# Optimization experiments

Measured on AMD Instinct MI355X. Metric: run time of the kernel, lower is better.

The kernel has to match this reference:

```python
import jax, jax.numpy as jnp
import numpy as np

B, C, H, W = 4, 64, 64, 64
C8 = C // 8


def cl_attention(x, gamma):
    # DANet CAM-style channel attention: [B,C,H,W] -> [B,C,H,W]
    b, c, h, w = x.shape
    xf = x.reshape(b, c, h * w)                       # b c n
    energy = jnp.einsum('bcn,bdn->bcd', xf, xf)       # b c c
    energy = jnp.max(energy, axis=-1, keepdims=True) - energy
    attn = jax.nn.softmax(energy, axis=-1)
    out = jnp.einsum('bcd,bdn->bcn', attn, xf).reshape(b, c, h, w)
    return gamma * out + x


def setup_inputs() -> dict:
    key = jax.random.key(0)
    ks = jax.random.split(key, 8)
    s = 0.02
    return {
        'cnn_feat': jax.random.normal(ks[0], (B, C, H, W), jnp.float32),
        'vit_feat': jax.random.normal(ks[1], (B, C, H, W), jnp.float32),
        'Wq': jax.random.normal(ks[2], (C8, C), jnp.float32) * s,   # 1x1 conv kernel
        'bq': jnp.zeros((C8,), jnp.float32),
        'Wk': jax.random.normal(ks[3], (C8, C), jnp.float32) * s,
        'bk': jnp.zeros((C8,), jnp.float32),
        'Wv': jax.random.normal(ks[4], (C, C), jnp.float32) * s,
        'bv': jnp.zeros((C,), jnp.float32),
        'gamma': jnp.zeros((1,), jnp.float32),
        'gamma_cla_cnn': jnp.zeros((1,), jnp.float32),
        'gamma_cla_vit': jnp.zeros((1,), jnp.float32),
    }


def reference(cnn_feat, vit_feat, Wq, bq, Wk, bk, Wv, bv, gamma,
              gamma_cla_cnn, gamma_cla_vit):
    b, c, h, w = cnn_feat.shape
    n = h * w

    cnn_att = cl_attention(cnn_feat, gamma_cla_cnn)   # b c h w
    vit_att = cl_attention(vit_feat, gamma_cla_vit)   # b c h w

    # query: 1x1 conv -> view(b, C8, n) -> permute -> (b, n, C8)
    q = jnp.einsum('bchw,oc->bhwo', cnn_att, Wq).reshape(b, n, -1) + bq

    # vit: rearrange 'b c h w -> b (h w) c'
    vit_flat = vit_att.reshape(b, c, n).transpose(0, 2, 1)          # b n c
    k = vit_flat @ Wk.T + bk                                        # b n C8
    v = vit_flat @ Wv.T + bv                                        # b n C

    energy = jnp.einsum('bqd,bkd->bqk', q, k)                       # b n n
    attn = jax.nn.softmax(energy, axis=-1)
    out = jnp.einsum('bqk,bkc->bqc', attn, v)                       # b n c
    out = out.transpose(0, 2, 1).reshape(b, c, h, w)                # 'b (h w) c -> b c h w'
    return gamma * out + cnn_feat
```

## Files before the change

### kernel.cpp

```cpp
#include <hip/hip_runtime.h>
#include <hip/hip_bf16.h>

#define BSZ 4
#define CC 64
#define NN 4096
#define CN (CC*NN)
#define BCN (BSZ*CN)

typedef __attribute__((ext_vector_type(4))) float    f4v;
typedef __attribute__((ext_vector_type(4))) int      i4v;
typedef __attribute__((ext_vector_type(2))) int      i2v;
typedef __attribute__((ext_vector_type(8))) short    s8v;

#define DPP_F(x_, ctrl_) __builtin_bit_cast(float, \
    __builtin_amdgcn_update_dpp(0, __builtin_bit_cast(int, (float)(x_)), (ctrl_), 0xf, 0xf, true))
#define QP_X1 0xB1

__device__ __forceinline__ unsigned pack_bf16(float lo, float hi) {
    unsigned l = __builtin_bit_cast(unsigned, lo);
    unsigned h = __builtin_bit_cast(unsigned, hi);
    return (h & 0xFFFF0000u) | (l >> 16);
}
__device__ __forceinline__ unsigned pack2(float lo, float hi) {
    float2 f2; f2.x = lo; f2.y = hi;
    __hip_bfloat162 h = __float22bfloat162_rn(f2);
    unsigned u;
    __builtin_memcpy(&u, &h, 4);
    return u;
}

__global__ __launch_bounds__(256) void gram_k(const float* __restrict__ cnn,
                                              const float* __restrict__ vit,
                                              float* __restrict__ part) {
    __shared__ __align__(16) float sXT[64*68];
    int t = threadIdx.x;
    int blk = blockIdx.x;
    int ch = blk & 63, b = (blk >> 6) & 3, i2 = blk >> 8;
    const float* X = (i2 ? vit : cnn) + b * CN;
    int n0 = ch * 64;
#pragma unroll
    for (int j = 0; j < 4; j++) {
        int idx = t + j * 256;
        int c = idx >> 4, n4 = idx & 15;
        f4v val = *(const f4v*)&X[c * NN + n0 + n4 * 4];
        int base = (n4 * 4) * 68 + c;
        sXT[base]       = val[0];
        sXT[base + 68]  = val[1];
        sXT[base + 136] = val[2];
        sXT[base + 204] = val[3];
    }
    __syncthreads();
    int tc = (t & 15) * 4, td = (t >> 4) * 4;
    f4v acc[4];
#pragma unroll
    for (int i = 0; i < 4; i++) acc[i] = (f4v){0.f, 0.f, 0.f, 0.f};
    for (int k = 0; k < 64; k++) {
        f4v a  = *(const f4v*)&sXT[k * 68 + tc];
        f4v bb = *(const f4v*)&sXT[k * 68 + td];
#pragma unroll
        for (int i = 0; i < 4; i++) acc[i] += a[i] * bb;
    }
    float* dst = part + ch * 32768 + (i2 * 4 + b) * 4096;
#pragma unroll
    for (int i = 0; i < 4; i++) *(f4v*)&dst[(tc + i) * 64 + td] = acc[i];
}

__global__ void gred_k(const float* __restrict__ part, float* __restrict__ G) {
    int row = blockIdx.x;
    int d = threadIdx.x;
    float s = 0.f;
#pragma unroll 8
    for (int ch = 0; ch < 64; ch++) s += part[ch * 32768 + row * 64 + d];
    float mn = s;
#pragma unroll
    for (int off = 1; off < 64; off <<= 1) mn = fminf(mn, __shfl_xor(mn, off));
    float e = __expf(mn - s);
    float sm = e;
#pragma unroll
    for (int off = 1; off < 64; off <<= 1) sm += __shfl_xor(sm, off);
    G[row * 64 + d] = e / sm;
}

__global__ __launch_bounds__(256) void weff_k(const float* __restrict__ G,
                                              const float* __restrict__ Wq,
                                              const float* __restrict__ Wk,
                                              const float* __restrict__ Wv,
                                              const float* __restrict__ gcnn,
                                              const float* __restrict__ gvit,
                                              ushort* __restrict__ WeffB) {
    __shared__ float sA[8192];
    __shared__ float sWt[1024];
    int t = threadIdx.x;
    int b = blockIdx.x / 5, tile = blockIdx.x % 5;
    for (int i = t; i < 4096; i += 256) {
        sA[i]        = G[b * 4096 + i];
        sA[4096 + i] = G[(4 + b) * 4096 + i];
    }
    __syncthreads();
    float gc = *gcnn, gv = *gvit;
#pragma unroll
    for (int k = 0; k < 4; k++) {
        int idx = k * 256 + t;
        int r = idx >> 6, c = idx & 63;
        const float* Wrow; const float* A; float g;
        if (tile == 0) {
            if (r < 8) { Wrow = Wq + r * 64;       A = sA;        g = gc; }
            else       { Wrow = Wk + (r - 8) * 64; A = sA + 4096; g = gv; }
        } else         { Wrow = Wv + ((tile - 1) * 16 + r) * 64; A = sA + 4096; g = gv; }
        float s = 0.f;
#pragma unroll 8
        for (int d = 0; d < 64; d++) s += Wrow[d] * A[d * 64 + c];
        sWt[idx] = g * s + Wrow[c];
    }
    __syncthreads();
    if (t < 128) {
        int frag = t >> 6, lane = t & 63, m = lane & 15, q4 = lane >> 4;
        i4v o;
#pragma unroll
        for (int p = 0; p < 4; p++) {
            int c0 = frag * 32 + q4 * 8 + 2 * p;
            o[p] = (int)pack_bf16(sWt[m * 64 + c0], sWt[m * 64 + c0 + 1]);
        }
        *(i4v*)&WeffB[(size_t)(b * 10 + tile * 2 + frag) * 512 + lane * 8] = o;
    }
}

__global__ __launch_bounds__(256) void qkv_k(const float* __restrict__ cnn,
                                             const float* __restrict__ vit,
                                             const ushort* __restrict__ WeffB,
                                             const float* __restrict__ bq,
                                             const float* __restrict__ bk,
                                             const float* __restrict__ bv,
                                             ushort* __restrict__ qb, ushort* __restrict__ kb,
                                             ushort* __restrict__ vT) {
    int t = threadIdx.x;
    int b = blockIdx.x >> 6, n0 = (blockIdx.x & 63) * 64;
    int w = t >> 6, lane = t & 63, c15 = lane & 15, q4 = lane >> 4;
    int n = n0 + w * 16 + c15;
    const float LOG2E = 1.44269504f;

    s8v A[10];
    const ushort* WB = WeffB + (size_t)b * 5120 + lane * 8;
#pragma unroll
    for (int i = 0; i < 10; i++)
        A[i] = __builtin_bit_cast(s8v, *(const i4v*)(WB + (size_t)i * 512));

    s8v Bc[2], Bv[2];
#pragma unroll
    for (int f = 0; f < 2; f++) {
        i4v pc, pv;
#pragma unroll
        for (int p = 0; p < 4; p++) {
            int c0 = f * 32 + q4 * 8 + p * 2;
            size_t a0 = (size_t)b * CN + (size_t)c0 * NN + n;
            pc[p] = (int)pack_bf16(cnn[a0], cnn[a0 + NN]);
            pv[p] = (int)pack_bf16(vit[a0], vit[a0 + NN]);
        }
        Bc[f] = __builtin_bit_cast(s8v, pc);
        Bv[f] = __builtin_bit_cast(s8v, pv);
    }

    f4v acc = *(const f4v*)(bq + (q4 & 1) * 4);
    acc = __builtin_amdgcn_mfma_f32_16x16x32_bf16(A[0], Bc[0], acc, 0, 0, 0);
    acc = __builtin_amdgcn_mfma_f32_16x16x32_bf16(A[1], Bc[1], acc, 0, 0, 0);
    if (q4 < 2) {
        unsigned d0 = pack_bf16(acc[0] * LOG2E, acc[1] * LOG2E);
        unsigned d1 = pack_bf16(acc[2] * LOG2E, acc[3] * LOG2E);
        unsigned long long v = ((unsigned long long)d1 << 32) | d0;
        *(unsigned long long*)&qb[(size_t)(b * NN + n) * 8 + q4 * 4] = v;
    }
    acc = *(const f4v*)(bk + (q4 & 1) * 4);
    acc = __builtin_amdgcn_mfma_f32_16x16x32_bf16(A[0], Bv[0], acc, 0, 0, 0);
    acc = __builtin_amdgcn_mfma_f32_16x16x32_bf16(A[1], Bv[1], acc, 0, 0, 0);
    if (q4 >= 2) {
        unsigned d0 = pack_bf16(acc[0], acc[1]), d1 = pack_bf16(acc[2], acc[3]);
        unsigned long long v = ((unsigned long long)d1 << 32) | d0;
        *(unsigned long long*)&kb[(size_t)(b * NN + n) * 8 + (q4 - 2) * 4] = v;
    }
#pragma unroll
    for (int tile = 1; tile < 5; tile++) {
        acc = *(const f4v*)(bv + (tile - 1) * 16 + q4 * 4);
        acc = __builtin_amdgcn_mfma_f32_16x16x32_bf16(A[tile * 2],     Bv[0], acc, 0, 0, 0);
        acc = __builtin_amdgcn_mfma_f32_16x16x32_bf16(A[tile * 2 + 1], Bv[1], acc, 0, 0, 0);
#pragma unroll
        for (int r = 0; r < 4; r++) {
            float other = DPP_F(acc[r], QP_X1);
            unsigned pkd = (lane & 1) ? pack_bf16(other, acc[r])
                                      : pack_bf16(acc[r], other);
            if (!(lane & 1)) {
                int row = (tile - 1) * 16 + q4 * 4 + r;
                *(unsigned*)&vT[(size_t)(b * 64 + row) * NN + n] = pkd;
            }
        }
    }
}

__global__ __launch_bounds__(256, 2) void flash_k(const ushort* __restrict__ qb,
                                                  const ushort* __restrict__ kb,
                                                  const ushort* __restrict__ vT,
                                                  float* __restrict__ pOT,
                                                  float* __restrict__ pl) {
    __shared__ __align__(16) ushort Vlds[64 * 72];
    int t = threadIdx.x;
    int lane = t & 63, w = t >> 6;
    int c15 = lane & 15, q4 = lane >> 4;
    int blk = blockIdx.x;
    int s = blk >> 6, b = (blk >> 4) & 3, q0 = (blk & 15) * 256;

    s8v qB[4];
#pragma unroll
    for (int g = 0; g < 4; g++) {
        i4v qa = (i4v){0, 0, 0, 0};
        if (q4 == 0)
            qa = *(const i4v*)(qb + (size_t)(b * NN + q0 + w * 64 + g * 16 + c15) * 8);
        qB[g] = __builtin_bit_cast(s8v, qa);
    }

    f4v accO[4][4];
#pragma unroll
    for (int g = 0; g < 4; g++)
#pragma unroll
        for (int nt = 0; nt < 4; nt++) accO[g][nt] = (f4v){0.f, 0.f, 0.f, 0.f};
    float lacc[4] = {0.f, 0.f, 0.f, 0.f};

    const ushort* kbb = kb + (size_t)b * NN * 8 + (size_t)c15 * 8;

    int r = t >> 2, chk = t & 3;
    const ushort* vsrc = vT + (size_t)(b * 64 + r) * NN + chk * 16;
    ushort* vdst = Vlds + r * 72 + 32 * (chk >> 1) + 4 * (chk & 1);

    int kbase = s * 512;
    i4v bk_cur[4];
#pragma unroll
    for (int nt = 0; nt < 4; nt++)
        bk_cur[nt] = *(const i4v*)(kbb + (size_t)(kbase + nt * 16) * 8);
    i4v v0 = *(const i4v*)(vsrc + kbase);
    i4v v1 = *(const i4v*)(vsrc + kbase + 8);

    for (int kt = 0; kt < 8; kt++) {
        int k0 = kbase + kt * 64;
        if (kt) __syncthreads();
        *(i2v*)(vdst + 0)  = (i2v){v0[0], v0[1]};
        *(i2v*)(vdst + 8)  = (i2v){v0[2], v0[3]};
        *(i2v*)(vdst + 16) = (i2v){v1[0], v1[1]};
        *(i2v*)(vdst + 24) = (i2v){v1[2], v1[3]};
        __syncthreads();

        i4v vA[2][4];
#pragma unroll
        for (int F = 0; F < 2; F++)
#pragma unroll
            for (int nt = 0; nt < 4; nt++)
                vA[F][nt] = *(const i4v*)(Vlds + (nt * 16 + c15) * 72 +
                                          32 * F + 8 * q4);

        i4v bk_nxt[4];
        if (kt < 7) {
            v0 = *(const i4v*)(vsrc + k0 + 64);
            v1 = *(const i4v*)(vsrc + k0 + 64 + 8);
#pragma unroll
            for (int nt = 0; nt < 4; nt++)
                bk_nxt[nt] = *(const i4v*)(kbb + (size_t)(k0 + 64 + nt * 16) * 8);
        }

#pragma unroll
        for (int gp = 0; gp < 2; gp++) {
            f4v z = (f4v){0.f, 0.f, 0.f, 0.f};
            f4v S[2][4];
#pragma unroll
            for (int gg = 0; gg < 2; gg++)
#pragma unroll
                for (int nt = 0; nt < 4; nt++)
                    S[gg][nt] = __builtin_amdgcn_mfma_f32_16x16x32_bf16(
                        __builtin_bit_cast(s8v, bk_cur[nt]), qB[gp * 2 + gg],
                        z, 0, 0, 0);

            s8v Bp[2][2];
#pragma unroll
            for (int gg = 0; gg < 2; gg++) {
                f4v p[4];
                float ps = 0.f;
#pragma unroll
                for (int nt = 0; nt < 4; nt++)
#pragma unroll
                    for (int rr = 0; rr < 4; rr++) {
                        p[nt][rr] = __builtin_amdgcn_exp2f(S[gg][nt][rr]);
                        ps += p[nt][rr];
                    }
#pragma unroll
                for (int F = 0; F < 2; F++) {
                    i4v bp;
                    bp[0] = (int)pack2(p[2 * F][0],     p[2 * F][1]);
                    bp[1] = (int)pack2(p[2 * F][2],     p[2 * F][3]);
                    bp[2] = (int)pack2(p[2 * F + 1][0], p[2 * F + 1][1]);
                    bp[3] = (int)pack2(p[2 * F + 1][2], p[2 * F + 1][3]);
                    Bp[gg][F] = __builtin_bit_cast(s8v, bp);
                }
                lacc[gp * 2 + gg] += ps;
            }

#pragma unroll
            for (int F = 0; F < 2; F++)
#pragma unroll
                for (int gg = 0; gg < 2; gg++)
#pragma unroll
                    for (int nt = 0; nt < 4; nt++)
                        accO[gp * 2 + gg][nt] =
                            __builtin_amdgcn_mfma_f32_16x16x32_bf16(
                                __builtin_bit_cast(s8v, vA[F][nt]), Bp[gg][F],
                                accO[gp * 2 + gg][nt], 0, 0, 0);
        }
        if (kt < 7) {
#pragma unroll
            for (int nt = 0; nt < 4; nt++) bk_cur[nt] = bk_nxt[nt];
        }
    }

#pragma unroll
    for (int g = 0; g < 4; g++) {
        lacc[g] += __shfl_xor(lacc[g], 16);
        lacc[g] += __shfl_xor(lacc[g], 32);
    }

#pragma unroll
    for (int g = 0; g < 4; g++) {
        int qg = q0 + w * 64 + g * 16 + c15;
#pragma unroll
        for (int nt = 0; nt < 4; nt++)
#pragma unroll
            for (int rr = 0; rr < 4; rr++) {
                int c = nt * 16 + q4 * 4 + rr;
                pOT[(size_t)((s * 4 + b) * 64 + c) * NN + qg] = accO[g][nt][rr];
            }
        if (q4 == 0)
            pl[(size_t)(s * 4 + b) * NN + qg] = lacc[g];
    }
}

__global__ __launch_bounds__(256) void comb_k(const float* __restrict__ pOT,
                                              const float* __restrict__ pl,
                                              const float* __restrict__ cnn,
                                              const float* __restrict__ gamma,
                                              float* __restrict__ out) {
    int t = threadIdx.x;
    int b = blockIdx.x >> 6, n0 = (blockIdx.x & 63) * 64;
    int nq = t & 15, cl = t >> 4;
    int n = n0 + nq * 4;
    f4v L = (f4v){0.f, 0.f, 0.f, 0.f};
#pragma unroll
    for (int s = 0; s < 8; s++)
        L += *(const f4v*)&pl[(size_t)(s * 4 + b) * NN + n];
    float g = *gamma;
    f4v rv;
#pragma unroll
    for (int j = 0; j < 4; j++) rv[j] = g / L[j];
#pragma unroll
    for (int it = 0; it < 4; it++) {
        int c = it * 16 + cl;
        f4v o = (f4v){0.f, 0.f, 0.f, 0.f};
#pragma unroll
        for (int s = 0; s < 8; s++)
            o += *(const f4v*)&pOT[(size_t)((s * 4 + b) * 64 + c) * NN + n];
        size_t gi = (size_t)(b * 64 + c) * NN + n;
        f4v cv = *(const f4v*)&cnn[gi];
        *(f4v*)&out[gi] = o * rv + cv;
    }
}

extern "C" void kernel_launch(void* const* d_in, const int* in_sizes, int n_in,
                              void* d_out, int out_size, void* d_ws, size_t ws_size,
                              hipStream_t stream) {
    const float* cnn  = (const float*)d_in[0];
    const float* vit  = (const float*)d_in[1];
    const float* Wq   = (const float*)d_in[2];
    const float* bq   = (const float*)d_in[3];
    const float* Wk   = (const float*)d_in[4];
    const float* bk   = (const float*)d_in[5];
    const float* Wv   = (const float*)d_in[6];
    const float* bv   = (const float*)d_in[7];
    const float* gam  = (const float*)d_in[8];
    const float* gcnn = (const float*)d_in[9];
    const float* gvit = (const float*)d_in[10];
    float* out = (float*)d_out;

    float* ws = (float*)d_ws;
    float*  pOT   = ws;
    float*  part  = ws;
    float*  G     = ws + 8388608;
    ushort* WeffB = (ushort*)(ws + 8421376);
    ushort* qb    = (ushort*)(ws + 8431616);
    ushort* kb    = (ushort*)(ws + 8497152);
    ushort* vT    = (ushort*)(ws + 8562688);
    float*  pl    = ws + 9086976;

    gram_k <<<512, 256, 0, stream>>>(cnn, vit, part);
    gred_k <<<512, 64,  0, stream>>>(part, G);
    weff_k <<<20,  256, 0, stream>>>(G, Wq, Wk, Wv, gcnn, gvit, WeffB);
    qkv_k  <<<256, 256, 0, stream>>>(cnn, vit, WeffB, bq, bk, bv, qb, kb, vT);
    flash_k<<<512, 256, 0, stream>>>(qb, kb, vT, pOT, pl);
    comb_k <<<256, 256, 0, stream>>>(pOT, pl, cnn, gam, out);
}
```

Before: 133.4 us.

## Store flash partial outputs as packed bf16 and double-buffer V tiles in LDS

The flash kernel now writes its per-split partial outputs as bf16, packed in a channel-quad interleaved layout, so each lane issues one 8-byte store per tile instead of scattered fp32 scalar stores. The combine kernel reads and unpacks those bf16 partials, roughly halving partial-buffer traffic. Separately, the V tile in LDS is double-buffered, which removes one barrier per K iteration. The cost is bf16 rounding of partial sums before the reduction across splits, plus twice the LDS use.

```diff
diff --git a/kernel.cpp b/kernel.cpp
--- a/kernel.cpp
+++ b/kernel.cpp
@@ -10,6 +10,7 @@
 typedef __attribute__((ext_vector_type(4))) float    f4v;
 typedef __attribute__((ext_vector_type(4))) int      i4v;
 typedef __attribute__((ext_vector_type(2))) int      i2v;
+typedef __attribute__((ext_vector_type(2))) unsigned u2v;
 typedef __attribute__((ext_vector_type(8))) short    s8v;
 
 #define DPP_F(x_, ctrl_) __builtin_bit_cast(float, \
@@ -27,6 +28,12 @@
     unsigned u;
     __builtin_memcpy(&u, &h, 4);
     return u;
+}
+__device__ __forceinline__ float blo(int d) {
+    return __builtin_bit_cast(float, (unsigned)d << 16);
+}
+__device__ __forceinline__ float bhi(int d) {
+    return __builtin_bit_cast(float, (unsigned)d & 0xFFFF0000u);
 }
 
 __global__ __launch_bounds__(256) void gram_k(const float* __restrict__ cnn,
@@ -198,9 +205,9 @@
 __global__ __launch_bounds__(256, 2) void flash_k(const ushort* __restrict__ qb,
                                                   const ushort* __restrict__ kb,
                                                   const ushort* __restrict__ vT,
-                                                  float* __restrict__ pOT,
+                                                  ushort* __restrict__ pOT,
                                                   float* __restrict__ pl) {
-    __shared__ __align__(16) ushort Vlds[64 * 72];
+    __shared__ __align__(16) ushort Vlds[2 * 64 * 72];
     int t = threadIdx.x;
     int lane = t & 63, w = t >> 6;
     int c15 = lane & 15, q4 = lane >> 4;
@@ -227,7 +234,8 @@
 
     int r = t >> 2, chk = t & 3;
     const ushort* vsrc = vT + (size_t)(b * 64 + r) * NN + chk * 16;
-    ushort* vdst = Vlds + r * 72 + 32 * (chk >> 1) + 4 * (chk & 1);
+    int vdstoff = r * 72 + 32 * (chk >> 1) + 4 * (chk & 1);
+    int vreadoff = c15 * 72 + 8 * q4;
 
     int kbase = s * 512;
     i4v bk_cur[4];
@@ -239,20 +247,20 @@
 
     for (int kt = 0; kt < 8; kt++) {
         int k0 = kbase + kt * 64;
-        if (kt) __syncthreads();
-        *(i2v*)(vdst + 0)  = (i2v){v0[0], v0[1]};
-        *(i2v*)(vdst + 8)  = (i2v){v0[2], v0[3]};
-        *(i2v*)(vdst + 16) = (i2v){v1[0], v1[1]};
-        *(i2v*)(vdst + 24) = (i2v){v1[2], v1[3]};
+        ushort* vd = Vlds + (kt & 1) * 4608 + vdstoff;
+        *(i2v*)(vd + 0)  = (i2v){v0[0], v0[1]};
+        *(i2v*)(vd + 8)  = (i2v){v0[2], v0[3]};
+        *(i2v*)(vd + 16) = (i2v){v1[0], v1[1]};
+        *(i2v*)(vd + 24) = (i2v){v1[2], v1[3]};
         __syncthreads();
 
+        const ushort* vb = Vlds + (kt & 1) * 4608 + vreadoff;
         i4v vA[2][4];
 #pragma unroll
         for (int F = 0; F < 2; F++)
 #pragma unroll
             for (int nt = 0; nt < 4; nt++)
-                vA[F][nt] = *(const i4v*)(Vlds + (nt * 16 + c15) * 72 +
-                                          32 * F + 8 * q4);
+                vA[F][nt] = *(const i4v*)(vb + nt * 16 * 72 + 32 * F);
 
         i4v bk_nxt[4];
         if (kt < 7) {
@@ -326,18 +334,19 @@
     for (int g = 0; g < 4; g++) {
         int qg = q0 + w * 64 + g * 16 + c15;
 #pragma unroll
-        for (int nt = 0; nt < 4; nt++)
-#pragma unroll
-            for (int rr = 0; rr < 4; rr++) {
-                int c = nt * 16 + q4 * 4 + rr;
-                pOT[(size_t)((s * 4 + b) * 64 + c) * NN + qg] = accO[g][nt][rr];
-            }
+        for (int nt = 0; nt < 4; nt++) {
+            int cg = nt * 4 + q4;
+            u2v d;
+            d[0] = pack2(accO[g][nt][0], accO[g][nt][1]);
+            d[1] = pack2(accO[g][nt][2], accO[g][nt][3]);
+            *(u2v*)&pOT[((size_t)((s * 4 + b) * 16 + cg) * NN + qg) * 4] = d;
+        }
         if (q4 == 0)
             pl[(size_t)(s * 4 + b) * NN + qg] = lacc[g];
     }
 }
 
-__global__ __launch_bounds__(256) void comb_k(const float* __restrict__ pOT,
+__global__ __launch_bounds__(256) void comb_k(const ushort* __restrict__ pOT,
                                               const float* __restrict__ pl,
                                               const float* __restrict__ cnn,
                                               const float* __restrict__ gamma,
@@ -354,16 +363,29 @@
     f4v rv;
 #pragma unroll
     for (int j = 0; j < 4; j++) rv[j] = g / L[j];
-#pragma unroll
-    for (int it = 0; it < 4; it++) {
-        int c = it * 16 + cl;
-        f4v o = (f4v){0.f, 0.f, 0.f, 0.f};
-#pragma unroll
-        for (int s = 0; s < 8; s++)
-            o += *(const f4v*)&pOT[(size_t)((s * 4 + b) * 64 + c) * NN + n];
-        size_t gi = (size_t)(b * 64 + c) * NN + n;
+
+    f4v Oc[4];
+#pragma unroll
+    for (int cc = 0; cc < 4; cc++) Oc[cc] = (f4v){0.f, 0.f, 0.f, 0.f};
+#pragma unroll
+    for (int s = 0; s < 8; s++) {
+        const ushort* src = pOT + ((size_t)((s * 4 + b) * 16 + cl) * NN + n) * 4;
+        i4v a  = *(const i4v*)src;
+        i4v bb = *(const i4v*)(src + 8);
+        Oc[0][0] += blo(a[0]);  Oc[1][0] += bhi(a[0]);
+        Oc[2][0] += blo(a[1]);  Oc[3][0] += bhi(a[1]);
+        Oc[0][1] += blo(a[2]);  Oc[1][1] += bhi(a[2]);
+        Oc[2][1] += blo(a[3]);  Oc[3][1] += bhi(a[3]);
+        Oc[0][2] += blo(bb[0]); Oc[1][2] += bhi(bb[0]);
+        Oc[2][2] += blo(bb[1]); Oc[3][2] += bhi(bb[1]);
+        Oc[0][3] += blo(bb[2]); Oc[1][3] += bhi(bb[2]);
+        Oc[2][3] += blo(bb[3]); Oc[3][3] += bhi(bb[3]);
+    }
+#pragma unroll
+    for (int cc = 0; cc < 4; cc++) {
+        size_t gi = (size_t)(b * 64 + cl * 4 + cc) * NN + n;
         f4v cv = *(const f4v*)&cnn[gi];
-        *(f4v*)&out[gi] = o * rv + cv;
+        *(f4v*)&out[gi] = Oc[cc] * rv + cv;
     }
 }
 
@@ -384,7 +406,7 @@
     float* out = (float*)d_out;
 
     float* ws = (float*)d_ws;
-    float*  pOT   = ws;
+    ushort* pOT   = (ushort*)ws;
     float*  part  = ws;
     float*  G     = ws + 8388608;
     ushort* WeffB = (ushort*)(ws + 8421376);
```

New measurement: 129.4 us. 1.03x faster.
